# Optimization experiments

Measured on AMD Instinct MI355X. Metric: run time of the kernel, lower is better.

## Reference

```python
import jax, jax.numpy as jnp
import numpy as np

EMBED_DIM = 1024
HEADS = 16
HEAD_DIM = EMBED_DIM // HEADS
N, SEQ = 2, 2048


def setup_inputs() -> dict:
    key = jax.random.key(0)
    ks = jax.random.split(key, 9)
    s = 1.0 / np.sqrt(HEAD_DIM)
    inp = {
        "values": jax.random.normal(ks[0], (N, SEQ, EMBED_DIM), jnp.float32),
        "keys": jax.random.normal(ks[1], (N, SEQ, EMBED_DIM), jnp.float32),
        "query": jax.random.normal(ks[2], (N, SEQ, EMBED_DIM), jnp.float32),
        "mask": jax.random.randint(ks[3], (N, 1, SEQ, SEQ), 0, 2, jnp.int32),
        # per-head projection weights (torch Linear: y = x @ W.T)
        "Wv": jax.random.normal(ks[4], (HEAD_DIM, HEAD_DIM), jnp.float32) * s,
        "Wk": jax.random.normal(ks[5], (HEAD_DIM, HEAD_DIM), jnp.float32) * s,
        "Wq": jax.random.normal(ks[6], (HEAD_DIM, HEAD_DIM), jnp.float32) * s,
        "Wo": jax.random.normal(ks[7], (EMBED_DIM, EMBED_DIM), jnp.float32) * (1.0 / np.sqrt(EMBED_DIM)),
        "bo": jax.random.normal(ks[8], (EMBED_DIM,), jnp.float32) * 0.01,
    }
    return inp


def reference(values, keys, query, mask, Wv, Wk, Wq, Wo, bo):
    n, q_len = query.shape[0], query.shape[1]
    v_len, k_len = values.shape[1], keys.shape[1]
    # reshape to [N, len, H, D]
    v = values.reshape(n, v_len, HEADS, HEAD_DIM)
    k = keys.reshape(n, k_len, HEADS, HEAD_DIM)
    q = query.reshape(n, q_len, HEADS, HEAD_DIM)
    # per-head linear projections (shared weight across heads), torch: x @ W.T
    v = jnp.einsum("nlhd,ed->nlhe", v, Wv)
    k = jnp.einsum("nlhd,ed->nlhe", k, Wk)
    q = jnp.einsum("nlhd,ed->nlhe", q, Wq)
    # energy: [N, H, Q, K]
    energy = jnp.einsum("nqhd,nkhd->nhqk", q, k)
    energy = jnp.where(mask == 0, jnp.float32(-1e20), energy)
    # NOTE: original scales by sqrt(embed_dim), not sqrt(head_dim)
    attention = jax.nn.softmax(energy / jnp.sqrt(jnp.float32(EMBED_DIM)), axis=3)
    out = jnp.einsum("nhql,nlhd->nqhd", attention, v).reshape(n, q_len, EMBED_DIM)
    out = out @ Wo.T + bo  # fc_out; dropout is identity in eval mode
    return out
```

## Files before the change

### kernel.cpp

```cpp
#include <hip/hip_runtime.h>
#include <hip/hip_bf16.h>

#define NB 2
#define SEQ 2048
#define HEADS 16
#define HD 64
#define ED 1024

typedef __bf16 bf16x8 __attribute__((ext_vector_type(8)));
typedef float f32x4 __attribute__((ext_vector_type(4)));
typedef unsigned short u16x8 __attribute__((ext_vector_type(8)));
typedef unsigned short u16x4 __attribute__((ext_vector_type(4)));

#if __has_builtin(__builtin_amdgcn_exp2f)
#define EXP2(x) __builtin_amdgcn_exp2f(x)
#else
#define EXP2(x) __builtin_exp2f(x)
#endif

__device__ __forceinline__ unsigned short f2bf(float f) {
    unsigned u = __builtin_bit_cast(unsigned, f);
    u += 0x7fffu + ((u >> 16) & 1u);
    return (unsigned short)(u >> 16);
}

__device__ __forceinline__ bf16x8 cvt8(const float* __restrict__ p) {
    const float4* p4 = (const float4*)p;
    float4 a = p4[0], b = p4[1];
    u16x8 u;
    u[0] = f2bf(a.x); u[1] = f2bf(a.y); u[2] = f2bf(a.z); u[3] = f2bf(a.w);
    u[4] = f2bf(b.x); u[5] = f2bf(b.y); u[6] = f2bf(b.z); u[7] = f2bf(b.w);
    return __builtin_bit_cast(bf16x8, u);
}

__device__ __forceinline__ bf16x8 ldfrag(const void* p) {
    uint4 v = *(const uint4*)p;
    return __builtin_bit_cast(bf16x8, v);
}

__device__ __forceinline__ f32x4 mfma16(bf16x8 a, bf16x8 b, f32x4 c) {
    return __builtin_amdgcn_mfma_f32_16x16x32_bf16(a, b, c, 0, 0, 0);
}

__device__ __forceinline__ unsigned packbf(float lo, float hi) {
    unsigned a = __builtin_bit_cast(unsigned, hi) + 0x8000u;
    unsigned b = __builtin_bit_cast(unsigned, lo) + 0x8000u;
    return __builtin_amdgcn_perm(a, b, 0x07060302u);
}

#define GLOAD_LDS(gp, lp) \
    __builtin_amdgcn_global_load_lds( \
        (const __attribute__((address_space(1))) unsigned int*)(gp), \
        (__attribute__((address_space(3))) unsigned int*)(lp), 16, 0, 0)

#define QSCALE 0.04508422f

__global__ __launch_bounds__(256) void proj_prep_kernel(
    const float* __restrict__ qin, const float* __restrict__ kin, const float* __restrict__ vin,
    const float* __restrict__ Wq, const float* __restrict__ Wk, const float* __restrict__ Wv,
    unsigned short* __restrict__ Qb, unsigned short* __restrict__ Kb,
    unsigned short* __restrict__ Vt,
    const int* __restrict__ mask, unsigned long long* __restrict__ bits,
    const float* __restrict__ Wo, unsigned short* __restrict__ Wob)
{
    __shared__ __align__(16) char tile[64 * 144];

    int bid = blockIdx.x;
    if (bid >= 3072) {
        int b2 = bid - 3072;
        if (b2 < NB * SEQ * SEQ / 256) {
            size_t i = (size_t)b2 * 256 + threadIdx.x;
            int m = mask[i];
            unsigned long long b = __ballot(m != 0);
            if ((threadIdx.x & 63) == 0) bits[i >> 6] = b;
        } else {
            size_t i = ((size_t)(b2 - NB * SEQ * SEQ / 256) * 256 + threadIdx.x) * 4;
            float4 v = *(const float4*)(Wo + i);
            u16x4 u;
            u[0] = f2bf(v.x); u[1] = f2bf(v.y); u[2] = f2bf(v.z); u[3] = f2bf(v.w);
            *(u16x4*)(Wob + i) = u;
        }
        return;
    }

    int t3  = bid >> 10;
    int rem = bid & 1023;
    int h   = rem >> 6;
    int rt  = rem & 63;
    int wave = threadIdx.x >> 6, lane = threadIdx.x & 63;
    int quad = lane >> 4, l16 = lane & 15;

    const float* in = (t3 == 0) ? qin : ((t3 == 1) ? kin : vin);
    const float* W  = (t3 == 0) ? Wq  : ((t3 == 1) ? Wk  : Wv);

    int r0 = rt * 64 + wave * 16;

    bf16x8 bf0[4], bf1[4];
#pragma unroll
    for (int sl = 0; sl < 4; ++sl) {
        const float* wrow = W + (sl * 16 + l16) * 64;
        bf0[sl] = cvt8(wrow + quad * 8);
        bf1[sl] = cvt8(wrow + 32 + quad * 8);
    }
    const float* xrow = in + (size_t)(r0 + l16) * ED + h * 64;
    bf16x8 af0 = cvt8(xrow + quad * 8);
    bf16x8 af1 = cvt8(xrow + 32 + quad * 8);

    f32x4 acc[4];
#pragma unroll
    for (int sl = 0; sl < 4; ++sl) {
        f32x4 c = {0.f, 0.f, 0.f, 0.f};
        c = mfma16(af0, bf0[sl], c);
        c = mfma16(af1, bf1[sl], c);
        acc[sl] = c;
    }
    float sc = (t3 == 0) ? QSCALE : 1.0f;

    size_t nh = (size_t)((r0 >> 11) * HEADS + h);
    int rl = lane >> 3, cl = lane & 7;

    if (t3 != 2) {
#pragma unroll
        for (int r = 0; r < 4; ++r) {
            int srow = wave * 16 + quad * 4 + r;
#pragma unroll
            for (int sl = 0; sl < 4; ++sl)
                *(unsigned short*)(tile + srow * 144 + (sl * 16 + l16) * 2) =
                    f2bf(acc[sl][r] * sc);
        }
        unsigned short* dst = (t3 == 0) ? Qb : Kb;
        int s0 = (r0 & 2047);
#pragma unroll
        for (int g = 0; g < 2; ++g) {
            int lrow = wave * 16 + g * 8 + rl;
            uint4 v = *(const uint4*)(tile + lrow * 144 + cl * 16);
            *(uint4*)(dst + (nh * SEQ + (s0 & ~15) + g * 8 + rl) * HD + cl * 8) = v;
        }
    } else {
#pragma unroll
        for (int r = 0; r < 4; ++r) {
            int srow = wave * 16 + quad * 4 + r;
#pragma unroll
            for (int sl = 0; sl < 4; ++sl)
                *(unsigned short*)(tile + (sl * 16 + l16) * 144 + srow * 2) =
                    f2bf(acc[sl][r]);
        }
        __syncthreads();
        int s_tile = rt & 31;
#pragma unroll
        for (int g = 0; g < 2; ++g) {
            int erow = wave * 16 + g * 8 + rl;
            uint4 v = *(const uint4*)(tile + erow * 144 + cl * 16);
            *(uint4*)(Vt + ((nh * 32 + s_tile) * 64 + erow) * 64 + cl * 8) = v;
        }
    }
}

__global__ __launch_bounds__(256, 4) void attn_kernel(
    const unsigned short* __restrict__ Qb, const unsigned short* __restrict__ Kb,
    const unsigned short* __restrict__ Vt2, const unsigned long long* __restrict__ mb,
    unsigned short* __restrict__ Ab)
{
    __shared__ __align__(16) char smem[32768 + 4 * 2048];

    int tid = threadIdx.x;
    int wave = tid >> 6, lane = tid & 63;
    int quad = lane >> 4, l16 = lane & 15;

    int b   = blockIdx.x;
    int xcd = b & 7;
    int j   = b >> 3;
    int nh  = xcd * 4 + (j >> 5);
    int qb  = j & 31;
    int n = nh >> 4, h = nh & 15;
    int q0 = qb * 64 + wave * 16;

    size_t headoff = (size_t)nh * SEQ * HD;
    const unsigned short* qrow = Qb + headoff + (size_t)(q0 + l16) * HD;
    bf16x8 qf0 = ldfrag(qrow + quad * 8);
    bf16x8 qf1 = ldfrag(qrow + 32 + quad * 8);

    int srow = lane >> 3, sslot = lane & 7;
    int stoff = srow * 128 + (((sslot - srow) & 7) * 16);

    int rotA = ((quad + l16) & 7) * 16;
    int aKV = l16 * 128 + rotA;

    int pswz = (l16 & 7) << 4;
    char* prow = smem + 32768 + wave * 2048 + l16 * 128;
    int pwoff = (quad * 8) ^ pswz;
    int proff = (quad * 16) ^ pswz;

    const unsigned short* gK = Kb + headoff;
    const unsigned short* gV = Vt2 + (size_t)nh * (32 * 4096);
    const unsigned long long* mbase = mb + (size_t)n * (SEQ * SEQ / 64)
                                         + (size_t)(q0 + l16) * (SEQ / 64);

    u16x8 ou;
#pragma unroll
    for (int jj = 0; jj < 8; ++jj) ou[jj] = 0x3F80;
    bf16x8 ones = __builtin_bit_cast(bf16x8, ou);

    f32x4 o[4] = {{0,0,0,0},{0,0,0,0},{0,0,0,0},{0,0,0,0}};
    f32x4 lacc = {0,0,0,0};
    int qsh = quad * 4;

    {
        const char* sK = (const char*)gK + stoff;
        const char* sV = (const char*)gV + stoff;
#pragma unroll
        for (int i2 = 0; i2 < 2; ++i2) {
            int c = wave * 2 + i2;
            GLOAD_LDS(sK + c * 1024, smem + c * 1024);
            GLOAD_LDS(sV + c * 1024, smem + 16384 + c * 1024);
        }
    }
    unsigned long long mnext = mbase[0] >> qsh;

    int par = 0;
    for (int kb = 0; kb < SEQ; kb += 64) {
        int kbn = (kb + 64) & (SEQ - 1);
        __syncthreads();
        {
            const char* sK = (const char*)(gK + (size_t)kbn * 64) + stoff;
            const char* sV = (const char*)(gV + (size_t)(kbn >> 6) * 4096) + stoff;
            char* dK = smem + (par ^ 1) * 8192;
            char* dV = smem + 16384 + (par ^ 1) * 8192;
#pragma unroll
            for (int i2 = 0; i2 < 2; ++i2) {
                int c = wave * 2 + i2;
                GLOAD_LDS(sK + c * 1024, dK + c * 1024);
                GLOAD_LDS(sV + c * 1024, dV + c * 1024);
            }
        }
        unsigned long long m64 = mnext;
        mnext = mbase[kbn >> 6] >> qsh;

        const char* kbuf = smem + par * 8192;
        bf16x8 kf[4][2];
#pragma unroll
        for (int kt = 0; kt < 4; ++kt) {
            kf[kt][0] = ldfrag(kbuf + aKV + kt * 2048);
            kf[kt][1] = ldfrag(kbuf + (aKV ^ 64) + kt * 2048);
        }
        f32x4 c[4];
#pragma unroll
        for (int kt = 0; kt < 4; ++kt) {
            f32x4 cc = {0.f, 0.f, 0.f, 0.f};
            cc = mfma16(kf[kt][0], qf0, cc);
            cc = mfma16(kf[kt][1], qf1, cc);
            c[kt] = cc;
        }
        unsigned mlo = (unsigned)m64;
        unsigned mhi = (unsigned)(m64 >> 32);
#pragma unroll
        for (int kt = 0; kt < 4; ++kt) {
            unsigned mw = (kt & 2) ? mhi : mlo;
            int bs = (kt & 1) ? 16 : 0;
            float p0 = ((mw >> (bs + 0)) & 1u) ? EXP2(c[kt][0]) : 0.f;
            float p1 = ((mw >> (bs + 1)) & 1u) ? EXP2(c[kt][1]) : 0.f;
            float p2 = ((mw >> (bs + 2)) & 1u) ? EXP2(c[kt][2]) : 0.f;
            float p3 = ((mw >> (bs + 3)) & 1u) ? EXP2(c[kt][3]) : 0.f;
            uint2 dw = { packbf(p0, p1), packbf(p2, p3) };
            *(uint2*)(prow + (pwoff ^ (kt * 32))) = dw;
        }
        bf16x8 pb0 = ldfrag(prow + proff);
        bf16x8 pb1 = ldfrag(prow + (proff ^ 64));
        lacc = mfma16(ones, pb0, lacc);
        lacc = mfma16(ones, pb1, lacc);
        const char* vbuf = smem + 16384 + par * 8192;
#pragma unroll
        for (int sl = 0; sl < 4; ++sl) {
            o[sl] = mfma16(ldfrag(vbuf + aKV + sl * 2048), pb0, o[sl]);
            o[sl] = mfma16(ldfrag(vbuf + (aKV ^ 64) + sl * 2048), pb1, o[sl]);
        }
        par ^= 1;
    }

    {
        float rinv = 1.0f / lacc[0];
        int q = q0 + l16;
        unsigned short* op = Ab + (((size_t)(n * SEQ + q)) * HEADS + h) * HD + qsh;
#pragma unroll
        for (int sl = 0; sl < 4; ++sl) {
            u16x4 u;
            u[0] = f2bf(o[sl][0] * rinv);
            u[1] = f2bf(o[sl][1] * rinv);
            u[2] = f2bf(o[sl][2] * rinv);
            u[3] = f2bf(o[sl][3] * rinv);
            *(u16x4*)(op + sl * 16) = u;
        }
    }
}

__global__ __launch_bounds__(256) void out_gemm_kernel(
    const unsigned short* __restrict__ Ab, const unsigned short* __restrict__ Wob,
    const float* __restrict__ bo, float* __restrict__ out)
{
    __shared__ __align__(16) char lds[49152];

    int tid = threadIdx.x;
    int wave = tid >> 6, lane = tid & 63;
    int quad = lane >> 4, l16 = lane & 15;
    int rt = blockIdx.x >> 4, ct = blockIdx.x & 15;
    int wr = wave >> 1, wc = wave & 1;

    int srow = lane >> 3, sslot = lane & 7;
    int stoff = srow * 2048 + (((sslot - srow) & 7) * 16);
    const char* gA = (const char*)Ab  + (size_t)rt * 128 * 2048 + stoff;
    const char* gB = (const char*)Wob + (size_t)ct * 64 * 2048 + stoff;

    int aA[4], aB[2];
#pragma unroll
    for (int i = 0; i < 4; ++i) {
        int rowA = wr * 64 + i * 16 + l16;
        aA[i] = rowA * 128 + (((quad + rowA) & 7) * 16);
    }
#pragma unroll
    for (int sl = 0; sl < 2; ++sl) {
        int rowB = wc * 32 + sl * 16 + l16;
        aB[sl] = rowB * 128 + (((quad + rowB) & 7) * 16);
    }

#pragma unroll
    for (int i = 0; i < 4; ++i) {
        int c = wave * 4 + i;
        GLOAD_LDS(gA + (size_t)c * 16384, lds + c * 1024);
    }
#pragma unroll
    for (int i = 0; i < 2; ++i) {
        int c = wave * 2 + i;
        GLOAD_LDS(gB + (size_t)c * 16384, lds + 32768 + c * 1024);
    }

    f32x4 acc[4][2] = {};
    int par = 0;
    for (int f = 0; f < ED; f += 64) {
        int fn = (f + 64) & (ED - 1);
        __syncthreads();
        {
            int pA = (par ^ 1) * 16384;
            int pB = 32768 + (par ^ 1) * 8192;
#pragma unroll
            for (int i = 0; i < 4; ++i) {
                int c = wave * 4 + i;
                GLOAD_LDS(gA + (size_t)c * 16384 + fn * 2, lds + pA + c * 1024);
            }
#pragma unroll
            for (int i = 0; i < 2; ++i) {
                int c = wave * 2 + i;
                GLOAD_LDS(gB + (size_t)c * 16384 + fn * 2, lds + pB + c * 1024);
            }
        }
        int bA = par * 16384;
        int bB = 32768 + par * 8192;
#pragma unroll
        for (int kk = 0; kk < 2; ++kk) {
            int x = kk * 64;
            bf16x8 af[4], bfr[2];
#pragma unroll
            for (int i = 0; i < 4; ++i)    af[i]  = ldfrag(lds + bA + (aA[i] ^ x));
#pragma unroll
            for (int sl = 0; sl < 2; ++sl) bfr[sl] = ldfrag(lds + bB + (aB[sl] ^ x));
#pragma unroll
            for (int i = 0; i < 4; ++i)
#pragma unroll
                for (int sl = 0; sl < 2; ++sl)
                    acc[i][sl] = mfma16(af[i], bfr[sl], acc[i][sl]);
        }
        par ^= 1;
    }

    float bv[2];
#pragma unroll
    for (int sl = 0; sl < 2; ++sl)
        bv[sl] = bo[ct * 64 + wc * 32 + sl * 16 + l16];
#pragma unroll
    for (int i = 0; i < 4; ++i)
#pragma unroll
        for (int r = 0; r < 4; ++r) {
            int row = rt * 128 + wr * 64 + i * 16 + quad * 4 + r;
#pragma unroll
            for (int sl = 0; sl < 2; ++sl) {
                int e = ct * 64 + wc * 32 + sl * 16 + l16;
                out[(size_t)row * ED + e] = acc[i][sl][r] + bv[sl];
            }
        }
}

extern "C" void kernel_launch(void* const* d_in, const int* in_sizes, int n_in,
                              void* d_out, int out_size, void* d_ws, size_t ws_size,
                              hipStream_t stream)
{
    const float* values = (const float*)d_in[0];
    const float* keys   = (const float*)d_in[1];
    const float* query  = (const float*)d_in[2];
    const int*   mask   = (const int*)d_in[3];
    const float* Wv     = (const float*)d_in[4];
    const float* Wk     = (const float*)d_in[5];
    const float* Wq     = (const float*)d_in[6];
    const float* Wo     = (const float*)d_in[7];
    const float* bo     = (const float*)d_in[8];
    float* out = (float*)d_out;

    char* w = (char*)d_ws;
    unsigned short* Qb  = (unsigned short*)(w);
    unsigned short* Kb  = (unsigned short*)(w +  8388608);
    unsigned short* Vt  = (unsigned short*)(w + 16777216);
    unsigned short* Ab  = (unsigned short*)(w + 25165824);
    unsigned long long* Mb = (unsigned long long*)(w + 33554432);
    unsigned short* Wob = (unsigned short*)(w + 34603008);

    proj_prep_kernel<<<3072 + NB * SEQ * SEQ / 256 + ED * ED / 1024, 256, 0, stream>>>(
        query, keys, values, Wq, Wk, Wv, Qb, Kb, Vt, mask, Mb, Wo, Wob);
    attn_kernel<<<1024, 256, 0, stream>>>(Qb, Kb, Vt, Mb, Ab);
    out_gemm_kernel<<<512, 256, 0, stream>>>(Ab, Wob, bo, out);
}
```

Measured before the change: 233.9 us.

## Process two query groups per wave to reuse K/V tiles across 128 queries

Each attention block now covers 128 query rows instead of 64, with every wave computing two 16-row groups against the same K/V fragments loaded from LDS. This halves the global K/V traffic and LDS fragment loads per query, and halves the grid size. The cost is more registers per wave, a lower occupancy bound, a doubled P staging buffer, and fewer blocks to spread across CUs.

```diff
diff --git a/kernel.cpp b/kernel.cpp
--- a/kernel.cpp
+++ b/kernel.cpp
@@ -156,12 +156,12 @@
     }
 }
 
-__global__ __launch_bounds__(256, 4) void attn_kernel(
+__global__ __launch_bounds__(256, 2) void attn_kernel(
     const unsigned short* __restrict__ Qb, const unsigned short* __restrict__ Kb,
     const unsigned short* __restrict__ Vt2, const unsigned long long* __restrict__ mb,
     unsigned short* __restrict__ Ab)
 {
-    __shared__ __align__(16) char smem[32768 + 4 * 2048];
+    __shared__ __align__(16) char smem[32768 + 4 * 4096];
 
     int tid = threadIdx.x;
     int wave = tid >> 6, lane = tid & 63;
@@ -170,15 +170,19 @@
     int b   = blockIdx.x;
     int xcd = b & 7;
     int j   = b >> 3;
-    int nh  = xcd * 4 + (j >> 5);
-    int qb  = j & 31;
+    int nh  = xcd * 4 + (j >> 4);
+    int qb  = j & 15;
     int n = nh >> 4, h = nh & 15;
-    int q0 = qb * 64 + wave * 16;
+    int q0 = qb * 128 + wave * 16;
 
     size_t headoff = (size_t)nh * SEQ * HD;
-    const unsigned short* qrow = Qb + headoff + (size_t)(q0 + l16) * HD;
-    bf16x8 qf0 = ldfrag(qrow + quad * 8);
-    bf16x8 qf1 = ldfrag(qrow + 32 + quad * 8);
+    bf16x8 qf[2][2];
+#pragma unroll
+    for (int g = 0; g < 2; ++g) {
+        const unsigned short* qrow = Qb + headoff + (size_t)(q0 + g * 64 + l16) * HD;
+        qf[g][0] = ldfrag(qrow + quad * 8);
+        qf[g][1] = ldfrag(qrow + 32 + quad * 8);
+    }
 
     int srow = lane >> 3, sslot = lane & 7;
     int stoff = srow * 128 + (((sslot - srow) & 7) * 16);
@@ -187,7 +191,8 @@
     int aKV = l16 * 128 + rotA;
 
     int pswz = (l16 & 7) << 4;
-    char* prow = smem + 32768 + wave * 2048 + l16 * 128;
+    char* prow0 = smem + 32768 + wave * 4096 + l16 * 128;
+    char* prow1 = prow0 + 2048;
     int pwoff = (quad * 8) ^ pswz;
     int proff = (quad * 16) ^ pswz;
 
@@ -201,8 +206,8 @@
     for (int jj = 0; jj < 8; ++jj) ou[jj] = 0x3F80;
     bf16x8 ones = __builtin_bit_cast(bf16x8, ou);
 
-    f32x4 o[4] = {{0,0,0,0},{0,0,0,0},{0,0,0,0},{0,0,0,0}};
-    f32x4 lacc = {0,0,0,0};
+    f32x4 o[2][4] = {};
+    f32x4 lacc[2] = {{0,0,0,0},{0,0,0,0}};
     int qsh = quad * 4;
 
     {
@@ -215,7 +220,8 @@
             GLOAD_LDS(sV + c * 1024, smem + 16384 + c * 1024);
         }
     }
-    unsigned long long mnext = mbase[0] >> qsh;
+    unsigned long long mnext0 = mbase[0] >> qsh;
+    unsigned long long mnext1 = mbase[2048] >> qsh;
 
     int par = 0;
     for (int kb = 0; kb < SEQ; kb += 64) {
@@ -233,8 +239,9 @@
                 GLOAD_LDS(sV + c * 1024, dV + c * 1024);
             }
         }
-        unsigned long long m64 = mnext;
-        mnext = mbase[kbn >> 6] >> qsh;
+        unsigned long long m64_0 = mnext0, m64_1 = mnext1;
+        mnext0 = mbase[kbn >> 6] >> qsh;
+        mnext1 = mbase[2048 + (kbn >> 6)] >> qsh;
 
         const char* kbuf = smem + par * 8192;
         bf16x8 kf[4][2];
@@ -243,51 +250,66 @@
             kf[kt][0] = ldfrag(kbuf + aKV + kt * 2048);
             kf[kt][1] = ldfrag(kbuf + (aKV ^ 64) + kt * 2048);
         }
-        f32x4 c[4];
-#pragma unroll
-        for (int kt = 0; kt < 4; ++kt) {
-            f32x4 cc = {0.f, 0.f, 0.f, 0.f};
-            cc = mfma16(kf[kt][0], qf0, cc);
-            cc = mfma16(kf[kt][1], qf1, cc);
-            c[kt] = cc;
-        }
-        unsigned mlo = (unsigned)m64;
-        unsigned mhi = (unsigned)(m64 >> 32);
-#pragma unroll
-        for (int kt = 0; kt < 4; ++kt) {
-            unsigned mw = (kt & 2) ? mhi : mlo;
-            int bs = (kt & 1) ? 16 : 0;
-            float p0 = ((mw >> (bs + 0)) & 1u) ? EXP2(c[kt][0]) : 0.f;
-            float p1 = ((mw >> (bs + 1)) & 1u) ? EXP2(c[kt][1]) : 0.f;
-            float p2 = ((mw >> (bs + 2)) & 1u) ? EXP2(c[kt][2]) : 0.f;
-            float p3 = ((mw >> (bs + 3)) & 1u) ? EXP2(c[kt][3]) : 0.f;
-            uint2 dw = { packbf(p0, p1), packbf(p2, p3) };
-            *(uint2*)(prow + (pwoff ^ (kt * 32))) = dw;
-        }
-        bf16x8 pb0 = ldfrag(prow + proff);
-        bf16x8 pb1 = ldfrag(prow + (proff ^ 64));
-        lacc = mfma16(ones, pb0, lacc);
-        lacc = mfma16(ones, pb1, lacc);
+#pragma unroll
+        for (int g = 0; g < 2; ++g) {
+            unsigned long long m64 = g ? m64_1 : m64_0;
+            char* prow = g ? prow1 : prow0;
+            f32x4 c[4];
+#pragma unroll
+            for (int kt = 0; kt < 4; ++kt) {
+                f32x4 cc = {0.f, 0.f, 0.f, 0.f};
+                cc = mfma16(kf[kt][0], qf[g][0], cc);
+                cc = mfma16(kf[kt][1], qf[g][1], cc);
+                c[kt] = cc;
+            }
+            unsigned mlo = (unsigned)m64;
+            unsigned mhi = (unsigned)(m64 >> 32);
+#pragma unroll
+            for (int kt = 0; kt < 4; ++kt) {
+                unsigned mw = (kt & 2) ? mhi : mlo;
+                int bs = (kt & 1) ? 16 : 0;
+                float p0 = ((mw >> (bs + 0)) & 1u) ? EXP2(c[kt][0]) : 0.f;
+                float p1 = ((mw >> (bs + 1)) & 1u) ? EXP2(c[kt][1]) : 0.f;
+                float p2 = ((mw >> (bs + 2)) & 1u) ? EXP2(c[kt][2]) : 0.f;
+                float p3 = ((mw >> (bs + 3)) & 1u) ? EXP2(c[kt][3]) : 0.f;
+                uint2 dw = { packbf(p0, p1), packbf(p2, p3) };
+                *(uint2*)(prow + (pwoff ^ (kt * 32))) = dw;
+            }
+        }
+        bf16x8 pb[2][2];
+        pb[0][0] = ldfrag(prow0 + proff);
+        pb[0][1] = ldfrag(prow0 + (proff ^ 64));
+        pb[1][0] = ldfrag(prow1 + proff);
+        pb[1][1] = ldfrag(prow1 + (proff ^ 64));
+        lacc[0] = mfma16(ones, pb[0][0], lacc[0]);
+        lacc[0] = mfma16(ones, pb[0][1], lacc[0]);
+        lacc[1] = mfma16(ones, pb[1][0], lacc[1]);
+        lacc[1] = mfma16(ones, pb[1][1], lacc[1]);
         const char* vbuf = smem + 16384 + par * 8192;
 #pragma unroll
         for (int sl = 0; sl < 4; ++sl) {
-            o[sl] = mfma16(ldfrag(vbuf + aKV + sl * 2048), pb0, o[sl]);
-            o[sl] = mfma16(ldfrag(vbuf + (aKV ^ 64) + sl * 2048), pb1, o[sl]);
+            bf16x8 va = ldfrag(vbuf + aKV + sl * 2048);
+            bf16x8 vx = ldfrag(vbuf + (aKV ^ 64) + sl * 2048);
+            o[0][sl] = mfma16(va, pb[0][0], o[0][sl]);
+            o[0][sl] = mfma16(vx, pb[0][1], o[0][sl]);
+            o[1][sl] = mfma16(va, pb[1][0], o[1][sl]);
+            o[1][sl] = mfma16(vx, pb[1][1], o[1][sl]);
         }
         par ^= 1;
     }
 
-    {
-        float rinv = 1.0f / lacc[0];
-        int q = q0 + l16;
+#pragma unroll
+    for (int g = 0; g < 2; ++g) {
+        float rinv = 1.0f / lacc[g][0];
+        int q = q0 + g * 64 + l16;
         unsigned short* op = Ab + (((size_t)(n * SEQ + q)) * HEADS + h) * HD + qsh;
 #pragma unroll
         for (int sl = 0; sl < 4; ++sl) {
             u16x4 u;
-            u[0] = f2bf(o[sl][0] * rinv);
-            u[1] = f2bf(o[sl][1] * rinv);
-            u[2] = f2bf(o[sl][2] * rinv);
-            u[3] = f2bf(o[sl][3] * rinv);
+            u[0] = f2bf(o[g][sl][0] * rinv);
+            u[1] = f2bf(o[g][sl][1] * rinv);
+            u[2] = f2bf(o[g][sl][2] * rinv);
+            u[3] = f2bf(o[g][sl][3] * rinv);
             *(u16x4*)(op + sl * 16) = u;
         }
     }
@@ -413,6 +435,6 @@
 
     proj_prep_kernel<<<3072 + NB * SEQ * SEQ / 256 + ED * ED / 1024, 256, 0, stream>>>(
         query, keys, values, Wq, Wk, Wv, Qb, Kb, Vt, mask, Mb, Wo, Wob);
-    attn_kernel<<<1024, 256, 0, stream>>>(Qb, Kb, Vt, Mb, Ab);
+    attn_kernel<<<512, 256, 0, stream>>>(Qb, Kb, Vt, Mb, Ab);
     out_gemm_kernel<<<512, 256, 0, stream>>>(Ab, Wob, bo, out);
 }
```

After: 236.3 us. About the same (+1.0%).
